# Optimization experiments

Hardware: AMD Instinct MI355X
Metric: run time of the kernel (lower is better)

## Reference

```python
import jax, jax.numpy as jnp
from jax import lax
import numpy as np


def setup_inputs() -> dict:
    key = jax.random.key(0)
    ks = jax.random.split(key, 8)
    B, Cin, H, W = 4, 64, 128, 128
    D, N = 2 * Cin, 64  # D = in_ch*2, N = ssd_state_dim*2
    s = np.float32(1.0 / np.sqrt(D))
    return {
        "x": jax.random.normal(ks[0], (B, Cin, H, W), jnp.float32),
        "h_prev": jnp.zeros((B, D, N), jnp.float32),
        "norm_w": jnp.ones((D,), jnp.float32),
        "norm_b": jnp.zeros((D,), jnp.float32),
        "W_x": jax.random.normal(ks[1], (D, D), jnp.float32) * s,
        "W_B": jax.random.normal(ks[2], (N, D), jnp.float32) * s,
        "W_C": jax.random.normal(ks[3], (N, D), jnp.float32) * s,
        "w_dt": jax.random.normal(ks[4], (D,), jnp.float32) * s,
        "dt_bias": jnp.float32(0.0),
        "A_log": jnp.float32(0.0),
        "D_skip": jax.random.normal(ks[5], (D,), jnp.float32),
        "W_out": jax.random.normal(ks[6], (D, D), jnp.float32) * s,
    }


def _forward(x, h_prev, norm_w, norm_b, W_x, W_B, W_C, w_dt, dt_bias, A_log, D_skip, W_out):
    B, C, H, W = x.shape
    # rfft2 -> complex [B, C, Hf, Wf]
    xf = jnp.fft.rfft2(x, norm='ortho')
    Hf, Wf = xf.shape[-2], xf.shape[-1]
    L = Hf * Wf
    sqrt_n = jnp.sqrt(jnp.float32(H * W))
    # pack real/imag along channels: [B, 2C, L]
    u = jnp.concatenate([xf.real.reshape(B, C, L), xf.imag.reshape(B, C, L)], axis=1)
    # LayerNorm1D over the channel dim
    mu = jnp.mean(u, axis=1, keepdims=True)
    var = jnp.var(u, axis=1, keepdims=True)
    u = (u - mu) * lax.rsqrt(var + 1e-5) * norm_w[None, :, None] + norm_b[None, :, None]
    u = u / sqrt_n
    # SSD (Mamba2-style) recurrence over the L frequency tokens
    xs = jnp.einsum('ed,bdl->lbe', W_x, u)   # [L, B, D]
    Bs = jnp.einsum('nd,bdl->lbn', W_B, u)   # [L, B, N]
    Cs = jnp.einsum('nd,bdl->lbn', W_C, u)   # [L, B, N]
    dt = jax.nn.softplus(jnp.einsum('d,bdl->lb', w_dt, u) + dt_bias)  # [L, B]
    dec = jnp.exp(-jnp.exp(A_log) * dt)       # [L, B], A = -exp(A_log)

    def step(h, inp):
        x_t, B_t, C_t, dec_t, dt_t = inp
        h = dec_t[:, None, None] * h + (dt_t[:, None] * x_t)[:, :, None] * B_t[:, None, :]
        y_t = jnp.einsum('bdn,bn->bd', h, C_t)
        return h, y_t

    h_last, ys = lax.scan(step, h_prev, (xs, Bs, Cs, dec, dt))  # ys [L, B, D]
    y = ys.transpose(1, 2, 0) + D_skip[None, :, None] * xs.transpose(1, 2, 0)  # [B, D, L]
    freq_out = jnp.einsum('ed,bdl->bel', W_out, y) * sqrt_n
    # unpack real/imag halves and inverse FFT
    ft = (freq_out[:, :C] + 1j * freq_out[:, C:]).reshape(B, C, Hf, Wf)
    y_sp = jnp.fft.irfft2(ft, s=(H, W), norm='ortho')
    return y_sp, h_last


def reference(x, h_prev, norm_w, norm_b, W_x, W_B, W_C, w_dt, dt_bias, A_log, D_skip, W_out):
    return _forward(x, h_prev, norm_w, norm_b, W_x, W_B, W_C, w_dt, dt_bias, A_log, D_skip, W_out)
```

## Files before the change

### kernel.cpp

```cpp
#include <hip/hip_runtime.h>
#include <hip/hip_bf16.h>
#include <math.h>

#define BB 4
#define CC 64
#define HH 128
#define WW 128
#define DD 128
#define NN 64
#define HF 128
#define WF 65
#define LL 8320
#define TSEG 64
#define NSEG 130
#define PI2f 6.283185307179586f

__device__ __forceinline__ int brev7(int x) { return (int)(__brev((unsigned)x) >> 25); }

__global__ void k0_transpose(const float* __restrict__ Wx, const float* __restrict__ Wb,
                             const float* __restrict__ Wc, const float* __restrict__ Wout,
                             float* __restrict__ WcatT, float* __restrict__ WoT) {
  int idx = blockIdx.x * 256 + threadIdx.x;
  if (idx < 128 * 256) {
    int k = idx >> 8, o = idx & 255;
    float v;
    if (o < 128)      v = Wx[o * 128 + k];
    else if (o < 192) v = Wb[(o - 128) * 128 + k];
    else              v = Wc[(o - 192) * 128 + k];
    WcatT[k * 256 + o] = v;
  }
  if (idx < 128 * 128) {
    int d = idx >> 7, e = idx & 127;
    WoT[d * 128 + e] = Wout[e * 128 + d];
  }
}

__global__ __launch_bounds__(256) void k1_rfft(const float* __restrict__ x,
                                               float* __restrict__ T1) {
  __shared__ float2 data[128 * 17];
  __shared__ float2 tw[64];
  int tid = threadIdx.x;
  if (tid < 64) {
    float sv, cv;
    sincosf(PI2f * (float)tid * (1.f / 128.f), &sv, &cv);
    tw[tid] = make_float2(cv, sv);
  }
  int r0 = blockIdx.x * 32;
  const float* xp = x + (size_t)r0 * 128;
#pragma unroll
  for (int i = 0; i < 8; i++) {
    int e = i * 256 + tid;
    int p = e >> 7, j = e & 127;
    float v1 = xp[(2 * p) * 128 + j];
    float v2 = xp[(2 * p + 1) * 128 + j];
    data[brev7(j) * 17 + p] = make_float2(v1, v2);
  }
  __syncthreads();
  for (int s = 1; s <= 7; s++) {
    int half = 1 << (s - 1);
    int tsh = 7 - s;
#pragma unroll
    for (int i = 0; i < 4; i++) {
      int idx = i * 256 + tid;
      int t = idx >> 4, c = idx & 15;
      int j = t & (half - 1);
      int pos = ((t >> (s - 1)) << s) + j;
      float2 a = data[pos * 17 + c];
      float2 b = data[(pos + half) * 17 + c];
      float2 w = tw[j << tsh];
      float2 m = make_float2(b.x * w.x + b.y * w.y, b.y * w.x - b.x * w.y);
      data[pos * 17 + c] = make_float2(a.x + m.x, a.y + m.y);
      data[(pos + half) * 17 + c] = make_float2(a.x - m.x, a.y - m.y);
    }
    __syncthreads();
  }
  const float inv = 1.f / 128.f;
  float2* o = (float2*)T1 + (size_t)r0 * 65;
#pragma unroll
  for (int i = 0; i < 5; i++) {
    int e = i * 256 + tid;
    if (e < 1040) {
      int p = e / 65, k = e - p * 65;
      float2 Z = data[k * 17 + p];
      float2 Zc = data[((128 - k) & 127) * 17 + p];
      float2 X1 = make_float2((Z.x + Zc.x) * 0.5f * inv, (Z.y - Zc.y) * 0.5f * inv);
      float2 X2 = make_float2((Z.y + Zc.y) * 0.5f * inv, (Zc.x - Z.x) * 0.5f * inv);
      o[(2 * p) * 65 + k] = X1;
      o[(2 * p + 1) * 65 + k] = X2;
    }
  }
}

__global__ __launch_bounds__(256) void k2a_fft(const float* __restrict__ T1,
                                               float* __restrict__ uT) {
  __shared__ float2 data[128 * 34];
  __shared__ float2 tw[64];
  int tid = threadIdx.x;
  if (tid < 64) {
    float sv, cv;
    sincosf(PI2f * (float)tid * (1.f / 128.f), &sv, &cv);
    tw[tid] = make_float2(cv, sv);
  }
  int chunk = blockIdx.x & 1;
  int bc = blockIdx.x >> 1;
  int wf0 = chunk * 32;
  const float2* Tp = (const float2*)T1 + (size_t)bc * 8320;
#pragma unroll
  for (int i = 0; i < 17; i++) {
    int e = i * 256 + tid;
    if (e < 4224) {
      int j = e / 33;
      int c = e - j * 33;
      data[brev7(j) * 34 + c] = Tp[j * 65 + wf0 + c];
    }
  }
  __syncthreads();
  for (int s = 1; s <= 7; s++) {
    int half = 1 << (s - 1);
    int tsh = 7 - s;
#pragma unroll
    for (int i = 0; i < 9; i++) {
      int idx = i * 256 + tid;
      if (idx < 2112) {
        int t = idx / 33;
        int c = idx - t * 33;
        int j = t & (half - 1);
        int pos = ((t >> (s - 1)) << s) + j;
        float2 a = data[pos * 34 + c];
        float2 b = data[(pos + half) * 34 + c];
        float2 w = tw[j << tsh];
        float2 m = make_float2(b.x * w.x + b.y * w.y, b.y * w.x - b.x * w.y);
        data[pos * 34 + c] = make_float2(a.x + m.x, a.y + m.y);
        data[(pos + half) * 34 + c] = make_float2(a.x - m.x, a.y - m.y);
      }
    }
    __syncthreads();
  }
  int b = bc >> 6, ch = bc & 63;
  float* pr = uT + (size_t)(b * 128 + ch) * 8320;
  float* pi = uT + (size_t)(b * 128 + 64 + ch) * 8320;
#pragma unroll
  for (int i = 0; i < 17; i++) {
    int e = i * 256 + tid;
    if (e < 4224) {
      int hf = e / 33;
      int c = e - hf * 33;
      float2 v = data[hf * 34 + c];
      pr[hf * 65 + wf0 + c] = v.x;
      pi[hf * 65 + wf0 + c] = v.y;
    }
  }
}

__global__ __launch_bounds__(512) void k3_ln_proj(
    const float* __restrict__ uT, const float* __restrict__ WcatT,
    const float* __restrict__ nw, const float* __restrict__ nb,
    const float* __restrict__ wdt, const float* __restrict__ dtbias,
    float* __restrict__ xs, float* __restrict__ Bs, float* __restrict__ Cs,
    float* __restrict__ dtb) {
  __shared__ float su[128 * 68];
  __shared__ float snw[128], snb[128], swdt[128];
  int tid = threadIdx.x;
  int b = blockIdx.x / 130, tile = blockIdx.x % 130;
  int l0 = tile * 64;
  if (tid < 128) { snw[tid] = nw[tid]; snb[tid] = nb[tid]; swdt[tid] = wdt[tid]; }
  const float* up = uT + (size_t)b * 128 * 8320 + l0;
#pragma unroll
  for (int i = 0; i < 4; i++) {
    int e = i * 512 + tid;
    int d = e >> 4, q = e & 15;
    float4 v = *(const float4*)(up + (size_t)d * 8320 + q * 4);
    *(float4*)&su[d * 68 + q * 4] = v;
  }
  __syncthreads();
  int t = tid >> 3, j = tid & 7;
  float vals[16];
  float s = 0.f, s2 = 0.f;
#pragma unroll
  for (int i = 0; i < 16; i++) {
    float v = su[(8 * i + j) * 68 + t];
    vals[i] = v; s += v; s2 += v * v;
  }
  s += __shfl_xor(s, 1, 64);  s += __shfl_xor(s, 2, 64);  s += __shfl_xor(s, 4, 64);
  s2 += __shfl_xor(s2, 1, 64); s2 += __shfl_xor(s2, 2, 64); s2 += __shfl_xor(s2, 4, 64);
  float mu = s * (1.f / 128.f);
  float var = s2 * (1.f / 128.f) - mu * mu;
  float rs = rsqrtf(var + 1e-5f);
  float raw = 0.f;
#pragma unroll
  for (int i = 0; i < 16; i++) {
    int k = 8 * i + j;
    float v = ((vals[i] - mu) * rs * snw[k] + snb[k]) * (1.f / 128.f);
    su[k * 68 + t] = v;
    raw = fmaf(v, swdt[k], raw);
  }
  raw += __shfl_xor(raw, 1, 64); raw += __shfl_xor(raw, 2, 64); raw += __shfl_xor(raw, 4, 64);
  if (j == 0) {
    float z = raw + dtbias[0];
    float sp = fmaxf(z, 0.f) + log1pf(expf(-fabsf(z)));
    dtb[b * LL + l0 + t] = sp;
  }
  __syncthreads();
  int wv = tid >> 6;
  int lane = tid & 63;
  int t0 = wv * 8;
  float acc[8][4];
#pragma unroll
  for (int i = 0; i < 8; i++)
#pragma unroll
    for (int r = 0; r < 4; r++) acc[i][r] = 0.f;
  const float4* W4 = (const float4*)WcatT;
  for (int k = 0; k < 128; k++) {
    float4 w = W4[k * 64 + lane];
    const float4* sr4 = (const float4*)&su[k * 68 + t0];
    float4 u0 = sr4[0], u1 = sr4[1];
    float uk[8] = {u0.x, u0.y, u0.z, u0.w, u1.x, u1.y, u1.z, u1.w};
#pragma unroll
    for (int i = 0; i < 8; i++) {
      acc[i][0] = fmaf(w.x, uk[i], acc[i][0]);
      acc[i][1] = fmaf(w.y, uk[i], acc[i][1]);
      acc[i][2] = fmaf(w.z, uk[i], acc[i][2]);
      acc[i][3] = fmaf(w.w, uk[i], acc[i][3]);
    }
  }
  size_t tok0 = (size_t)b * LL + l0 + t0;
  float* basep;
  size_t stride;
  if (lane < 32)      { basep = xs + tok0 * 128 + lane * 4;        stride = 128; }
  else if (lane < 48) { basep = Bs + tok0 * 64 + (lane - 32) * 4;  stride = 64; }
  else                { basep = Cs + tok0 * 64 + (lane - 48) * 4;  stride = 64; }
#pragma unroll
  for (int i = 0; i < 8; i++)
    *(float4*)(basep + (size_t)i * stride) =
        make_float4(acc[i][0], acc[i][1], acc[i][2], acc[i][3]);
}

__global__ __launch_bounds__(256) void k5_seg(
    const float* __restrict__ xs, const float* __restrict__ Bs, const float* __restrict__ Cs,
    const float* __restrict__ dtb, const float* __restrict__ Alog,
    const float* __restrict__ Dskip,
    float* __restrict__ ybuf, float* __restrict__ Sseg, float* __restrict__ ssegb,
    float* __restrict__ cumg) {
  __shared__ __align__(16) float sB[64 * 68];
  __shared__ __align__(16) float sCM[64 * 68];
  __shared__ float sdt[64], slc[64], sws[64];
  int tid = threadIdx.x;
  int b = blockIdx.x / NSEG, seg = blockIdx.x % NSEG;
  int tokbase = b * LL + seg * TSEG;
  const float4* xg = (const float4*)(xs + (size_t)tokbase * 128);
  const float4* bg = (const float4*)(Bs + (size_t)tokbase * 64);
  const float4* cg = (const float4*)(Cs + (size_t)tokbase * 64);
#pragma unroll
  for (int i = 0; i < 4; i++) {
    int e = i * 256 + tid;
    int t = e >> 4, n4 = e & 15;
    *(float4*)&sB[t * 68 + n4 * 4] = bg[e];
    *(float4*)&sCM[t * 68 + n4 * 4] = cg[e];
  }
  if (tid < 64) sdt[tid] = dtb[tokbase + tid];
  __syncthreads();
  if (tid < 64) {
    float a = expf(Alog[0]);
    float v = -a * sdt[tid];
#pragma unroll
    for (int off = 1; off < 64; off <<= 1) {
      float o = __shfl_up(v, off, 64);
      if (tid >= off) v += o;
    }
    slc[tid] = v;
    float l63 = __shfl(v, 63, 64);
    sws[tid] = expf(l63 - v) * sdt[tid];
    cumg[tokbase + tid] = expf(v);
    if (tid == 63) ssegb[seg * BB + b] = expf(v);
  }
  __syncthreads();
  int t0 = (tid >> 4) * 4, s0 = (tid & 15) * 4;
  float g[4][4];
#pragma unroll
  for (int i = 0; i < 4; i++)
#pragma unroll
    for (int j = 0; j < 4; j++) g[i][j] = 0.f;
  for (int n4 = 0; n4 < 16; n4++) {
    float4 cr[4], br[4];
#pragma unroll
    for (int i = 0; i < 4; i++) cr[i] = *(const float4*)&sCM[(t0 + i) * 68 + n4 * 4];
#pragma unroll
    for (int j = 0; j < 4; j++) br[j] = *(const float4*)&sB[(s0 + j) * 68 + n4 * 4];
#pragma unroll
    for (int i = 0; i < 4; i++)
#pragma unroll
      for (int j = 0; j < 4; j++) {
        g[i][j] = fmaf(cr[i].x, br[j].x, g[i][j]);
        g[i][j] = fmaf(cr[i].y, br[j].y, g[i][j]);
        g[i][j] = fmaf(cr[i].z, br[j].z, g[i][j]);
        g[i][j] = fmaf(cr[i].w, br[j].w, g[i][j]);
      }
  }
  __syncthreads();
#pragma unroll
  for (int i = 0; i < 4; i++) {
    int t = t0 + i;
    float4 m;
    float lt = slc[t];
    m.x = (s0 + 0 <= t) ? expf(lt - slc[s0 + 0]) * sdt[s0 + 0] * g[i][0] : 0.f;
    m.y = (s0 + 1 <= t) ? expf(lt - slc[s0 + 1]) * sdt[s0 + 1] * g[i][1] : 0.f;
    m.z = (s0 + 2 <= t) ? expf(lt - slc[s0 + 2]) * sdt[s0 + 2] * g[i][2] : 0.f;
    m.w = (s0 + 3 <= t) ? expf(lt - slc[s0 + 3]) * sdt[s0 + 3] * g[i][3] : 0.f;
    *(float4*)&sCM[t * 68 + s0] = m;
  }
  __syncthreads();
  {
    int d4 = (tid & 15) * 2;
    float acc[4][8];
#pragma unroll
    for (int i = 0; i < 4; i++)
#pragma unroll
      for (int j = 0; j < 8; j++) acc[i][j] = 0.f;
    for (int s = 0; s < 64; s++) {
      float4 x0 = xg[s * 32 + d4];
      float4 x1 = xg[s * 32 + d4 + 1];
      float xv[8] = {x0.x, x0.y, x0.z, x0.w, x1.x, x1.y, x1.z, x1.w};
#pragma unroll
      for (int i = 0; i < 4; i++) {
        float m = sCM[(t0 + i) * 68 + s];
#pragma unroll
        for (int j = 0; j < 8; j++) acc[i][j] = fmaf(m, xv[j], acc[i][j]);
      }
    }
    int d0 = d4 * 4;
    float4 dk0 = *(const float4*)&Dskip[d0];
    float4 dk1 = *(const float4*)&Dskip[d0 + 4];
    float dk[8] = {dk0.x, dk0.y, dk0.z, dk0.w, dk1.x, dk1.y, dk1.z, dk1.w};
#pragma unroll
    for (int i = 0; i < 4; i++) {
      int t = t0 + i;
      float4 x0 = xg[t * 32 + d4];
      float4 x1 = xg[t * 32 + d4 + 1];
      float xv[8] = {x0.x, x0.y, x0.z, x0.w, x1.x, x1.y, x1.z, x1.w};
      float4 y0, y1;
      y0.x = fmaf(dk[0], xv[0], acc[i][0]); y0.y = fmaf(dk[1], xv[1], acc[i][1]);
      y0.z = fmaf(dk[2], xv[2], acc[i][2]); y0.w = fmaf(dk[3], xv[3], acc[i][3]);
      y1.x = fmaf(dk[4], xv[4], acc[i][4]); y1.y = fmaf(dk[5], xv[5], acc[i][5]);
      y1.z = fmaf(dk[6], xv[6], acc[i][6]); y1.w = fmaf(dk[7], xv[7], acc[i][7]);
      float* yp = ybuf + (size_t)(tokbase + t) * 128 + d0;
      *(float4*)yp = y0;
      *(float4*)(yp + 4) = y1;
    }
  }
  {
    int dd4 = (tid >> 4) * 2, n0 = (tid & 15) * 4;
    float sacc[8][4];
#pragma unroll
    for (int k = 0; k < 8; k++)
#pragma unroll
      for (int j = 0; j < 4; j++) sacc[k][j] = 0.f;
    for (int s = 0; s < 64; s++) {
      float w = sws[s];
      float4 b4 = *(const float4*)&sB[s * 68 + n0];
      b4.x *= w; b4.y *= w; b4.z *= w; b4.w *= w;
      float4 x0 = xg[s * 32 + dd4];
      float4 x1 = xg[s * 32 + dd4 + 1];
      float xv[8] = {x0.x, x0.y, x0.z, x0.w, x1.x, x1.y, x1.z, x1.w};
#pragma unroll
      for (int k = 0; k < 8; k++) {
        sacc[k][0] = fmaf(xv[k], b4.x, sacc[k][0]);
        sacc[k][1] = fmaf(xv[k], b4.y, sacc[k][1]);
        sacc[k][2] = fmaf(xv[k], b4.z, sacc[k][2]);
        sacc[k][3] = fmaf(xv[k], b4.w, sacc[k][3]);
      }
    }
    int dd0 = dd4 * 4;
    float* Sp = Sseg + (size_t)seg * 32768 + (size_t)b * 8192;
#pragma unroll
    for (int k = 0; k < 8; k++)
      *(float4*)&Sp[(dd0 + k) * 64 + n0] =
          make_float4(sacc[k][0], sacc[k][1], sacc[k][2], sacc[k][3]);
  }
}

__global__ void k5b_states(const float* __restrict__ h_prev, const float* __restrict__ Sseg,
                           const float* __restrict__ ssegb, float* __restrict__ Hp,
                           float* __restrict__ h_last) {
  int gid = blockIdx.x * 256 + threadIdx.x;
  int b = gid >> 13;
  float h = h_prev[gid];
  for (int p = 0; p < NSEG; p++) {
    Hp[(size_t)p * 32768 + gid] = h;
    h = fmaf(ssegb[p * 4 + b], h, Sseg[(size_t)p * 32768 + gid]);
  }
  h_last[gid] = h;
}

__global__ __launch_bounds__(512) void k5c_correct(
    const float* __restrict__ Cs, const float* __restrict__ Hp,
    const float* __restrict__ cumg, float* __restrict__ ybuf) {
  __shared__ __align__(16) float Ct[64 * 64];
  __shared__ __align__(16) float Ht[64 * 132];
  __shared__ float cg[64];
  int tid = threadIdx.x;
  int b = blockIdx.x / NSEG, seg = blockIdx.x % NSEG;
  int tokbase = b * LL + seg * 64;
  const float* Csrc = Cs + (size_t)tokbase * 64;
#pragma unroll
  for (int i = 0; i < 8; i++) {
    int e = tid + i * 512;
    Ct[(e & 63) * 64 + (e >> 6)] = Csrc[e];
  }
  const float* Hsrc = Hp + (size_t)seg * 32768 + (size_t)b * 8192;
#pragma unroll
  for (int i = 0; i < 16; i++) {
    int e = tid + i * 512;
    Ht[(e & 63) * 132 + (e >> 6)] = Hsrc[e];
  }
  if (tid < 64) cg[tid] = cumg[tokbase + tid];
  __syncthreads();
  int og = tid & 15, tg = tid >> 4;
  int d0 = og * 8, t0 = tg * 2;
  float acc[2][8];
#pragma unroll
  for (int i = 0; i < 2; i++)
#pragma unroll
    for (int jj = 0; jj < 8; jj++) acc[i][jj] = 0.f;
  for (int n = 0; n < 64; n++) {
    float2 c2 = *(const float2*)&Ct[n * 64 + t0];
    float4 h0 = *(const float4*)&Ht[n * 132 + d0];
    float4 h1 = *(const float4*)&Ht[n * 132 + d0 + 4];
    float cv[2] = {c2.x, c2.y};
    float hv[8] = {h0.x, h0.y, h0.z, h0.w, h1.x, h1.y, h1.z, h1.w};
#pragma unroll
    for (int i = 0; i < 2; i++)
#pragma unroll
      for (int jj = 0; jj < 8; jj++) acc[i][jj] = fmaf(cv[i], hv[jj], acc[i][jj]);
  }
#pragma unroll
  for (int i = 0; i < 2; i++) {
    float sc = cg[t0 + i];
    float* yp = ybuf + (size_t)(tokbase + t0 + i) * 128 + d0;
    float4 y0 = *(float4*)yp;
    float4 y1 = *(float4*)(yp + 4);
    y0.x = fmaf(sc, acc[i][0], y0.x); y0.y = fmaf(sc, acc[i][1], y0.y);
    y0.z = fmaf(sc, acc[i][2], y0.z); y0.w = fmaf(sc, acc[i][3], y0.w);
    y1.x = fmaf(sc, acc[i][4], y1.x); y1.y = fmaf(sc, acc[i][5], y1.y);
    y1.z = fmaf(sc, acc[i][6], y1.z); y1.w = fmaf(sc, acc[i][7], y1.w);
    *(float4*)yp = y0; *(float4*)(yp + 4) = y1;
  }
}

__global__ __launch_bounds__(512) void k6_outproj(
    const float* __restrict__ ybuf, const float* __restrict__ WoT,
    float* __restrict__ T2) {
  __shared__ float sy[128 * 68];
  int tid = threadIdx.x;
  int b = blockIdx.x / 130, tile = blockIdx.x % 130;
  int l0 = tile * 64;
  const float* yg = ybuf + ((size_t)b * LL + l0) * 128;
#pragma unroll
  for (int i = 0; i < 4; i++) {
    int e = i * 512 + tid;
    int t = e >> 5, q = e & 31;
    float4 v = *(const float4*)(yg + t * 128 + q * 4);
    sy[(q * 4 + 0) * 68 + t] = v.x; sy[(q * 4 + 1) * 68 + t] = v.y;
    sy[(q * 4 + 2) * 68 + t] = v.z; sy[(q * 4 + 3) * 68 + t] = v.w;
  }
  __syncthreads();
  int wv = tid >> 6;
  int lane = tid & 63;
  int o4 = lane & 31, th = lane >> 5;
  int tt0 = wv * 8 + th * 4;
  float acc[4][4];
#pragma unroll
  for (int i = 0; i < 4; i++)
#pragma unroll
    for (int r = 0; r < 4; r++) acc[i][r] = 0.f;
  const float4* W4 = (const float4*)WoT;
  for (int k = 0; k < 128; k++) {
    float4 w = W4[k * 32 + o4];
    const float4* sr4 = (const float4*)&sy[k * 68 + tt0];
    float4 u0 = sr4[0];
    float yk[4] = {u0.x, u0.y, u0.z, u0.w};
#pragma unroll
    for (int i = 0; i < 4; i++) {
      acc[i][0] = fmaf(w.x, yk[i], acc[i][0]);
      acc[i][1] = fmaf(w.y, yk[i], acc[i][1]);
      acc[i][2] = fmaf(w.z, yk[i], acc[i][2]);
      acc[i][3] = fmaf(w.w, yk[i], acc[i][3]);
    }
  }
#pragma unroll
  for (int i = 0; i < 4; i++) {
    int l = l0 + tt0 + i;
    *(float4*)(T2 + ((size_t)b * LL + l) * 128 + o4 * 4) =
        make_float4(acc[i][0] * 128.f, acc[i][1] * 128.f,
                    acc[i][2] * 128.f, acc[i][3] * 128.f);
  }
}

__global__ __launch_bounds__(256) void k7t_transpose(const float* __restrict__ T2,
                                                     float* __restrict__ T2T) {
  __shared__ __align__(16) float tile[32][132];
  int tid = threadIdx.x;
  int b = blockIdx.x / 260, lt = blockIdx.x % 260;
  int l0 = lt * 32;
#pragma unroll
  for (int i = 0; i < 4; i++) {
    int e = i * 256 + tid;
    int l = e >> 5, f4 = e & 31;
    float4 v = *(const float4*)(T2 + ((size_t)(b * LL + l0 + l)) * 128 + f4 * 4);
    *(float4*)&tile[l][f4 * 4] = v;
  }
  __syncthreads();
  int l = tid & 31, c2 = tid >> 5;
  float2* out = (float2*)T2T;
#pragma unroll
  for (int k = 0; k < 8; k++) {
    int c = c2 * 8 + k;
    float2 z = make_float2(tile[l][c], tile[l][64 + c]);
    out[((size_t)(b * 64 + c)) * 8320 + l0 + l] = z;
  }
}

__global__ __launch_bounds__(256) void k7a_fft(const float* __restrict__ T2T,
                                               float* __restrict__ TY) {
  __shared__ float2 data[128 * 34];
  __shared__ float2 tw[64];
  int tid = threadIdx.x;
  if (tid < 64) {
    float sv, cv;
    sincosf(PI2f * (float)tid * (1.f / 128.f), &sv, &cv);
    tw[tid] = make_float2(cv, sv);
  }
  int chunk = blockIdx.x & 1;
  int bc = blockIdx.x >> 1;
  int wf0 = chunk * 32;
  const float2* Zp = (const float2*)T2T + (size_t)bc * 8320;
#pragma unroll
  for (int i = 0; i < 17; i++) {
    int e = i * 256 + tid;
    if (e < 4224) {
      int j = e / 33;
      int c = e - j * 33;
      data[brev7(j) * 34 + c] = Zp[j * 65 + wf0 + c];
    }
  }
  __syncthreads();
  for (int s = 1; s <= 7; s++) {
    int half = 1 << (s - 1);
    int tsh = 7 - s;
#pragma unroll
    for (int i = 0; i < 9; i++) {
      int idx = i * 256 + tid;
      if (idx < 2112) {
        int t = idx / 33;
        int c = idx - t * 33;
        int j = t & (half - 1);
        int pos = ((t >> (s - 1)) << s) + j;
        float2 a = data[pos * 34 + c];
        float2 b = data[(pos + half) * 34 + c];
        float2 w = tw[j << tsh];
        float2 m = make_float2(b.x * w.x - b.y * w.y, b.y * w.x + b.x * w.y);
        data[pos * 34 + c] = make_float2(a.x + m.x, a.y + m.y);
        data[(pos + half) * 34 + c] = make_float2(a.x - m.x, a.y - m.y);
      }
    }
    __syncthreads();
  }
  float2* po = (float2*)TY + (size_t)bc * 8320;
#pragma unroll
  for (int i = 0; i < 17; i++) {
    int e = i * 256 + tid;
    if (e < 4224) {
      int h = e / 33;
      int c = e - h * 33;
      po[h * 65 + wf0 + c] = data[h * 34 + c];
    }
  }
}

__global__ __launch_bounds__(256) void k8_irfft(const float* __restrict__ TY,
                                                float* __restrict__ out) {
  __shared__ float2 zsh[32 * 66];
  __shared__ float2 data[128 * 17];
  __shared__ float2 tw[64];
  int tid = threadIdx.x;
  if (tid < 64) {
    float sv, cv;
    sincosf(PI2f * (float)tid * (1.f / 128.f), &sv, &cv);
    tw[tid] = make_float2(cv, sv);
  }
  int r0 = blockIdx.x * 32;
  const float2* Zp = (const float2*)TY + (size_t)r0 * 65;
#pragma unroll
  for (int i = 0; i < 9; i++) {
    int e = i * 256 + tid;
    if (e < 2080) {
      int r = e / 65, wf = e - r * 65;
      zsh[r * 66 + wf] = Zp[r * 65 + wf];
    }
  }
  __syncthreads();
#pragma unroll
  for (int i = 0; i < 8; i++) {
    int e = i * 256 + tid;
    int p = e >> 7, j = e & 127;
    int jj = (j <= 64) ? j : 128 - j;
    float2 a1 = zsh[(2 * p) * 66 + jj];
    float2 a2 = zsh[(2 * p + 1) * 66 + jj];
    if (jj == 0 || jj == 64) { a1.y = 0.f; a2.y = 0.f; }
    float2 V = (j <= 64) ? make_float2(a1.x - a2.y, a1.y + a2.x)
                         : make_float2(a1.x + a2.y, a2.x - a1.y);
    data[brev7(j) * 17 + p] = V;
  }
  __syncthreads();
  for (int s = 1; s <= 7; s++) {
    int half = 1 << (s - 1);
    int tsh = 7 - s;
#pragma unroll
    for (int i = 0; i < 4; i++) {
      int idx = i * 256 + tid;
      int t = idx >> 4, c = idx & 15;
      int j = t & (half - 1);
      int pos = ((t >> (s - 1)) << s) + j;
      float2 a = data[pos * 17 + c];
      float2 b = data[(pos + half) * 17 + c];
      float2 w = tw[j << tsh];
      float2 m = make_float2(b.x * w.x - b.y * w.y, b.y * w.x + b.x * w.y);
      data[pos * 17 + c] = make_float2(a.x + m.x, a.y + m.y);
      data[(pos + half) * 17 + c] = make_float2(a.x - m.x, a.y - m.y);
    }
    __syncthreads();
  }
  const float inv = 1.f / 128.f;
  float* op = out + (size_t)r0 * 128;
#pragma unroll
  for (int i = 0; i < 8; i++) {
    int e = i * 256 + tid;
    int p = e >> 7, w = e & 127;
    float2 X = data[w * 17 + p];
    op[(2 * p) * 128 + w] = X.x * inv;
    op[(2 * p + 1) * 128 + w] = X.y * inv;
  }
}

extern "C" void kernel_launch(void* const* d_in, const int* in_sizes, int n_in,
                              void* d_out, int out_size, void* d_ws, size_t ws_size,
                              hipStream_t stream) {
  const float* x      = (const float*)d_in[0];
  const float* h_prev = (const float*)d_in[1];
  const float* nw     = (const float*)d_in[2];
  const float* nb     = (const float*)d_in[3];
  const float* Wx     = (const float*)d_in[4];
  const float* Wb     = (const float*)d_in[5];
  const float* Wc     = (const float*)d_in[6];
  const float* wdt    = (const float*)d_in[7];
  const float* dtbias = (const float*)d_in[8];
  const float* Alog   = (const float*)d_in[9];
  const float* Dskip  = (const float*)d_in[10];
  const float* Wout   = (const float*)d_in[11];
  float* out = (float*)d_out;

  float* ws = (float*)d_ws;
  const size_t SZ_BIG = 4259840;
  const size_t SZ_BN  = 2129920;
  float* RA = ws;
  float* RB = RA + SZ_BIG;
  float* RC = RB + SZ_BIG;
  float* RD = RC + SZ_BIG;
  float* RE = RD + SZ_BN;
  float* dtb   = RE + SZ_BN;
  float* cumg  = dtb + 33280;
  float* ssegb = cumg + 33280;
  float* WcatT = ssegb + 520;
  float* WoT   = WcatT + 32768;

  hipLaunchKernelGGL(k0_transpose, dim3(128), dim3(256), 0, stream, Wx, Wb, Wc, Wout, WcatT, WoT);
  hipLaunchKernelGGL(k1_rfft, dim3(1024), dim3(256), 0, stream, x, RA );
  hipLaunchKernelGGL(k2a_fft, dim3(512), dim3(256), 0, stream, RA , RB );
  hipLaunchKernelGGL(k3_ln_proj, dim3(520), dim3(512), 0, stream,
                     RB , WcatT, nw, nb, wdt, dtbias, RA , RD , RE , dtb);
  hipLaunchKernelGGL(k5_seg, dim3(520), dim3(256), 0, stream,
                     RA , RD , RE , dtb, Alog, Dskip,
                     RB , RC , ssegb, cumg);
  hipLaunchKernelGGL(k5b_states, dim3(128), dim3(256), 0, stream,
                     h_prev, RC , ssegb, RA , out + 4194304);
  hipLaunchKernelGGL(k5c_correct, dim3(520), dim3(512), 0, stream,
                     RE , RA , cumg, RB );
  hipLaunchKernelGGL(k6_outproj, dim3(520), dim3(512), 0, stream, RB , WoT, RC );
  hipLaunchKernelGGL(k7t_transpose, dim3(1040), dim3(256), 0, stream, RC , RD );
  hipLaunchKernelGGL(k7a_fft, dim3(512), dim3(256), 0, stream, RD , RA );
  hipLaunchKernelGGL(k8_irfft, dim3(1024), dim3(256), 0, stream, RA , out);
}
```

Before: 218.4 us.

## Split segment SSD kernel into mask kernel and dual-task y/state kernel

Breaks the monolithic per-segment kernel into k5m, which computes the decayed C·B^T mask and writes it to a global buffer, and k5ys, which launches twice as many blocks, each doing either the intra-segment y product or the segment state accumulation. The goal is more parallelism, since 520 blocks with large shared-memory footprints underfill the GPU, and lower per-block shared memory. The cost is an extra launch, a global round trip for the 64x64 mask per segment, and a recomputed dt cumsum. The mask kernel now reads C and B tiles straight from global memory instead of staging them in LDS.

```diff
diff --git a/kernel.cpp b/kernel.cpp
--- a/kernel.cpp
+++ b/kernel.cpp
@@ -235,28 +235,14 @@
         make_float4(acc[i][0], acc[i][1], acc[i][2], acc[i][3]);
 }
 
-__global__ __launch_bounds__(256) void k5_seg(
-    const float* __restrict__ xs, const float* __restrict__ Bs, const float* __restrict__ Cs,
+__global__ __launch_bounds__(256) void k5m(
+    const float* __restrict__ Bs, const float* __restrict__ Cs,
     const float* __restrict__ dtb, const float* __restrict__ Alog,
-    const float* __restrict__ Dskip,
-    float* __restrict__ ybuf, float* __restrict__ Sseg, float* __restrict__ ssegb,
-    float* __restrict__ cumg) {
-  __shared__ __align__(16) float sB[64 * 68];
-  __shared__ __align__(16) float sCM[64 * 68];
-  __shared__ float sdt[64], slc[64], sws[64];
+    float* __restrict__ Mbuf, float* __restrict__ ssegb, float* __restrict__ cumg) {
+  __shared__ float sdt[64], slc[64];
   int tid = threadIdx.x;
   int b = blockIdx.x / NSEG, seg = blockIdx.x % NSEG;
   int tokbase = b * LL + seg * TSEG;
-  const float4* xg = (const float4*)(xs + (size_t)tokbase * 128);
-  const float4* bg = (const float4*)(Bs + (size_t)tokbase * 64);
-  const float4* cg = (const float4*)(Cs + (size_t)tokbase * 64);
-#pragma unroll
-  for (int i = 0; i < 4; i++) {
-    int e = i * 256 + tid;
-    int t = e >> 4, n4 = e & 15;
-    *(float4*)&sB[t * 68 + n4 * 4] = bg[e];
-    *(float4*)&sCM[t * 68 + n4 * 4] = cg[e];
-  }
   if (tid < 64) sdt[tid] = dtb[tokbase + tid];
   __syncthreads();
   if (tid < 64) {
@@ -268,13 +254,13 @@
       if (tid >= off) v += o;
     }
     slc[tid] = v;
-    float l63 = __shfl(v, 63, 64);
-    sws[tid] = expf(l63 - v) * sdt[tid];
     cumg[tokbase + tid] = expf(v);
     if (tid == 63) ssegb[seg * BB + b] = expf(v);
   }
   __syncthreads();
   int t0 = (tid >> 4) * 4, s0 = (tid & 15) * 4;
+  const float4* bg = (const float4*)(Bs + (size_t)tokbase * 64);
+  const float4* cg = (const float4*)(Cs + (size_t)tokbase * 64);
   float g[4][4];
 #pragma unroll
   for (int i = 0; i < 4; i++)
@@ -283,9 +269,9 @@
   for (int n4 = 0; n4 < 16; n4++) {
     float4 cr[4], br[4];
 #pragma unroll
-    for (int i = 0; i < 4; i++) cr[i] = *(const float4*)&sCM[(t0 + i) * 68 + n4 * 4];
-#pragma unroll
-    for (int j = 0; j < 4; j++) br[j] = *(const float4*)&sB[(s0 + j) * 68 + n4 * 4];
+    for (int i = 0; i < 4; i++) cr[i] = cg[(t0 + i) * 16 + n4];
+#pragma unroll
+    for (int j = 0; j < 4; j++) br[j] = bg[(s0 + j) * 16 + n4];
 #pragma unroll
     for (int i = 0; i < 4; i++)
 #pragma unroll
@@ -296,20 +282,43 @@
         g[i][j] = fmaf(cr[i].w, br[j].w, g[i][j]);
       }
   }
-  __syncthreads();
+  float* Mp = Mbuf + (size_t)blockIdx.x * 4096;
 #pragma unroll
   for (int i = 0; i < 4; i++) {
     int t = t0 + i;
+    float lt = slc[t];
     float4 m;
-    float lt = slc[t];
     m.x = (s0 + 0 <= t) ? expf(lt - slc[s0 + 0]) * sdt[s0 + 0] * g[i][0] : 0.f;
     m.y = (s0 + 1 <= t) ? expf(lt - slc[s0 + 1]) * sdt[s0 + 1] * g[i][1] : 0.f;
     m.z = (s0 + 2 <= t) ? expf(lt - slc[s0 + 2]) * sdt[s0 + 2] * g[i][2] : 0.f;
     m.w = (s0 + 3 <= t) ? expf(lt - slc[s0 + 3]) * sdt[s0 + 3] * g[i][3] : 0.f;
-    *(float4*)&sCM[t * 68 + s0] = m;
-  }
-  __syncthreads();
-  {
+    *(float4*)&Mp[t * 64 + s0] = m;
+  }
+}
+
+__global__ __launch_bounds__(256) void k5ys(
+    const float* __restrict__ xs, const float* __restrict__ Bs,
+    const float* __restrict__ dtb, const float* __restrict__ Alog,
+    const float* __restrict__ Dskip, const float* __restrict__ Mbuf,
+    float* __restrict__ ybuf, float* __restrict__ Sseg) {
+  __shared__ __align__(16) float sT[64 * 68];
+  __shared__ float sdt[64], sws[64];
+  int tid = threadIdx.x;
+  int task = blockIdx.x & 1;
+  int bs = blockIdx.x >> 1;
+  int b = bs / NSEG, seg = bs % NSEG;
+  int tokbase = b * LL + seg * TSEG;
+  const float4* xg = (const float4*)(xs + (size_t)tokbase * 128);
+  if (task == 0) {
+    const float4* mg = (const float4*)(Mbuf + (size_t)bs * 4096);
+#pragma unroll
+    for (int i = 0; i < 4; i++) {
+      int e = i * 256 + tid;
+      int t = e >> 4, q = e & 15;
+      *(float4*)&sT[t * 68 + q * 4] = mg[e];
+    }
+    __syncthreads();
+    int t0 = (tid >> 4) * 4;
     int d4 = (tid & 15) * 2;
     float acc[4][8];
 #pragma unroll
@@ -322,7 +331,7 @@
       float xv[8] = {x0.x, x0.y, x0.z, x0.w, x1.x, x1.y, x1.z, x1.w};
 #pragma unroll
       for (int i = 0; i < 4; i++) {
-        float m = sCM[(t0 + i) * 68 + s];
+        float m = sT[(t0 + i) * 68 + s];
 #pragma unroll
         for (int j = 0; j < 8; j++) acc[i][j] = fmaf(m, xv[j], acc[i][j]);
       }
@@ -346,8 +355,28 @@
       *(float4*)yp = y0;
       *(float4*)(yp + 4) = y1;
     }
-  }
-  {
+  } else {
+    const float4* bg = (const float4*)(Bs + (size_t)tokbase * 64);
+#pragma unroll
+    for (int i = 0; i < 4; i++) {
+      int e = i * 256 + tid;
+      int t = e >> 4, n4 = e & 15;
+      *(float4*)&sT[t * 68 + n4 * 4] = bg[e];
+    }
+    if (tid < 64) sdt[tid] = dtb[tokbase + tid];
+    __syncthreads();
+    if (tid < 64) {
+      float a = expf(Alog[0]);
+      float v = -a * sdt[tid];
+#pragma unroll
+      for (int off = 1; off < 64; off <<= 1) {
+        float o = __shfl_up(v, off, 64);
+        if (tid >= off) v += o;
+      }
+      float l63 = __shfl(v, 63, 64);
+      sws[tid] = expf(l63 - v) * sdt[tid];
+    }
+    __syncthreads();
     int dd4 = (tid >> 4) * 2, n0 = (tid & 15) * 4;
     float sacc[8][4];
 #pragma unroll
@@ -356,7 +385,7 @@
       for (int j = 0; j < 4; j++) sacc[k][j] = 0.f;
     for (int s = 0; s < 64; s++) {
       float w = sws[s];
-      float4 b4 = *(const float4*)&sB[s * 68 + n0];
+      float4 b4 = *(const float4*)&sT[s * 68 + n0];
       b4.x *= w; b4.y *= w; b4.z *= w; b4.w *= w;
       float4 x0 = xg[s * 32 + dd4];
       float4 x1 = xg[s * 32 + dd4 + 1];
@@ -671,15 +700,18 @@
   float* ssegb = cumg + 33280;
   float* WcatT = ssegb + 520;
   float* WoT   = WcatT + 32768;
+  float* Mbuf  = WoT + 16384;
 
   hipLaunchKernelGGL(k0_transpose, dim3(128), dim3(256), 0, stream, Wx, Wb, Wc, Wout, WcatT, WoT);
   hipLaunchKernelGGL(k1_rfft, dim3(1024), dim3(256), 0, stream, x, RA );
   hipLaunchKernelGGL(k2a_fft, dim3(512), dim3(256), 0, stream, RA , RB );
   hipLaunchKernelGGL(k3_ln_proj, dim3(520), dim3(512), 0, stream,
                      RB , WcatT, nw, nb, wdt, dtbias, RA , RD , RE , dtb);
-  hipLaunchKernelGGL(k5_seg, dim3(520), dim3(256), 0, stream,
-                     RA , RD , RE , dtb, Alog, Dskip,
-                     RB , RC , ssegb, cumg);
+  hipLaunchKernelGGL(k5m, dim3(520), dim3(256), 0, stream,
+                     RD , RE , dtb, Alog, Mbuf, ssegb, cumg);
+  hipLaunchKernelGGL(k5ys, dim3(1040), dim3(256), 0, stream,
+                     RA , RD , dtb, Alog, Dskip, Mbuf,
+                     RB , RC );
   hipLaunchKernelGGL(k5b_states, dim3(128), dim3(256), 0, stream,
                      h_prev, RC , ssegb, RA , out + 4194304);
   hipLaunchKernelGGL(k5c_correct, dim3(520), dim3(512), 0, stream,
```

New measurement: 248.0 us. 1.14x slower.
